# Optimization experiments

Measured on AMD Instinct MI355X. Metric: run time of the kernel, lower is better.

## Reference

```python
import jax, jax.numpy as jnp
import numpy as np

DIM = 1024
HEADS = 16
HEAD_DIM = DIM // HEADS
SCALE = HEAD_DIM ** -0.5


def setup_inputs() -> dict:
    key = jax.random.key(0)
    k1, k2, k3 = jax.random.split(key, 3)
    x = jax.random.normal(k1, (4, 2048, DIM), dtype=jnp.float32)
    # nn.Linear weight shape [out, in]; y = x @ W.T
    W_qkv = jax.random.normal(k2, (3 * DIM, DIM), dtype=jnp.float32) * (DIM ** -0.5)
    W_proj = jax.random.normal(k3, (DIM, DIM), dtype=jnp.float32) * (DIM ** -0.5)
    b_proj = jnp.zeros((DIM,), dtype=jnp.float32)
    return {"x": x, "W_qkv": W_qkv, "W_proj": W_proj, "b_proj": b_proj}


def reference(x, W_qkv, W_proj, b_proj):
    B, N, C = x.shape
    qkv = x @ W_qkv.T  # [B, N, 3C]
    qkv = qkv.reshape(B, N, 3, HEADS, HEAD_DIM).transpose(2, 0, 3, 1, 4)  # [3,B,H,N,D]
    q, k, v = qkv[0], qkv[1], qkv[2]
    attn = jnp.einsum('bhnd,bhmd->bhnm', q, k) * SCALE
    attn = jax.nn.softmax(attn, axis=-1)
    out = jnp.einsum('bhnm,bhmd->bhnd', attn, v)  # [B,H,N,D]
    out = out.transpose(0, 2, 1, 3).reshape(B, N, C)
    return out @ W_proj.T + b_proj
```

## Files before the change

kernel.cpp:

```cpp
#include <hip/hip_runtime.h>
#include <hip/hip_bf16.h>
#include <stdint.h>

typedef __attribute__((ext_vector_type(8))) __bf16 bf16x8;
typedef __attribute__((ext_vector_type(4))) float f32x4;
typedef __attribute__((ext_vector_type(16))) float f32x16;
typedef __attribute__((ext_vector_type(8))) unsigned short u16x8;
typedef __attribute__((ext_vector_type(4))) unsigned int u32x4;

#define DIM 1024
#define SEQ 2048
#define BATCH 4
#define MROWS (BATCH*SEQ)
#define QK_SCALE 0.1803368801111204f

__device__ __forceinline__ unsigned short f2bf(float f) {
  unsigned int u = __float_as_uint(f);
  u += 0x7fff + ((u >> 16) & 1);
  return (unsigned short)(u >> 16);
}

__device__ __forceinline__ void async16(const void* g, void* l) {
  __builtin_amdgcn_global_load_lds(
      (const __attribute__((address_space(1))) unsigned int*)g,
      (__attribute__((address_space(3))) unsigned int*)l, 16, 0, 0);
}

__device__ __forceinline__ unsigned cvtpk(float lo, float hi) {
  unsigned r;
  asm("v_cvt_pk_bf16_f32 %0, %1, %2" : "=v"(r) : "v"(lo), "v"(hi));
  return r;
}

__global__ __launch_bounds__(256) void cvt3(
    const float* __restrict__ x, const float* __restrict__ w1,
    const float* __restrict__ w2, unsigned short* __restrict__ xb,
    unsigned short* __restrict__ w1b, unsigned short* __restrict__ w2b) {
  const size_t NX = (size_t)MROWS * DIM;
  const size_t NW1 = (size_t)3 * DIM * DIM;
  const size_t NW2 = (size_t)DIM * DIM;
  size_t i = ((size_t)blockIdx.x * blockDim.x + threadIdx.x) * 8;
  const float* s; unsigned short* d; size_t off;
  if (i < NX) { s = x; d = xb; off = i; }
  else if (i < NX + NW1) { s = w1; d = w1b; off = i - NX; }
  else if (i < NX + NW1 + NW2) { s = w2; d = w2b; off = i - NX - NW1; }
  else return;
  float4 a = *(const float4*)(s + off);
  float4 b = *(const float4*)(s + off + 4);
  u16x8 r;
  r[0] = f2bf(a.x); r[1] = f2bf(a.y); r[2] = f2bf(a.z); r[3] = f2bf(a.w);
  r[4] = f2bf(b.x); r[5] = f2bf(b.y); r[6] = f2bf(b.z); r[7] = f2bf(b.w);
  *(u16x8*)(d + off) = r;
}

template<int OUT_BF16>
__global__ __launch_bounds__(256) void gemm_bt(
    const unsigned short* __restrict__ A, const unsigned short* __restrict__ Bt,
    unsigned short* __restrict__ Cb, float* __restrict__ Cf,
    const float* __restrict__ bias, int M, int N, int K,
    float qscale, int qcols)
{
  __shared__ unsigned short Asm[128 * 64];
  __shared__ unsigned short Bsm[128 * 64];

  int nwg = gridDim.x;
  int bid = blockIdx.x;
  int cpx = nwg >> 3;
  int wg = (bid & 7) * cpx + (bid >> 3);
  int ntn = N >> 7;
  int tn = wg % ntn, tm = wg / ntn;

  int t = threadIdx.x, l = t & 63, w = t >> 6;
  int lr = l & 15, lg = l >> 4;
  int wr = w >> 1, wc = w & 1;

  f32x4 acc[4][4] = {};

  const unsigned short* Ab = A + (size_t)tm * 128 * K;
  const unsigned short* Bb = Bt + (size_t)tn * 128 * K;

  for (int k0 = 0; k0 < K; k0 += 64) {
    #pragma unroll
    for (int i = 0; i < 4; ++i) {
      int idx = i * 256 + t;
      int row = idx >> 3, cc = (idx & 7) * 8;
      async16(Ab + (size_t)row * K + k0 + cc, (char*)Asm + idx * 16);
      async16(Bb + (size_t)row * K + k0 + cc, (char*)Bsm + idx * 16);
    }
    __syncthreads();
    #pragma unroll
    for (int kk = 0; kk < 2; ++kk) {
      bf16x8 af[4], bfr[4];
      #pragma unroll
      for (int m = 0; m < 4; ++m)
        af[m] = *(const bf16x8*)&Asm[(wr * 64 + m * 16 + lr) * 64 + kk * 32 + lg * 8];
      #pragma unroll
      for (int n = 0; n < 4; ++n)
        bfr[n] = *(const bf16x8*)&Bsm[(wc * 64 + n * 16 + lr) * 64 + kk * 32 + lg * 8];
      #pragma unroll
      for (int m = 0; m < 4; ++m)
        #pragma unroll
        for (int n = 0; n < 4; ++n)
          acc[m][n] = __builtin_amdgcn_mfma_f32_16x16x32_bf16(af[m], bfr[n], acc[m][n], 0, 0, 0);
    }
    __syncthreads();
  }

  #pragma unroll
  for (int m = 0; m < 4; ++m)
    #pragma unroll
    for (int n = 0; n < 4; ++n) {
      int col = tn * 128 + wc * 64 + n * 16 + lr;
      float cs = (OUT_BF16 && col < qcols) ? qscale : 1.0f;
      #pragma unroll
      for (int j = 0; j < 4; ++j) {
        int row = tm * 128 + wr * 64 + m * 16 + lg * 4 + j;
        if (OUT_BF16) Cb[(size_t)row * N + col] = f2bf(acc[m][n][j] * cs);
        else          Cf[(size_t)row * N + col] = acc[m][n][j] + bias[col];
      }
    }
}

__global__ __launch_bounds__(256, 4) void attn_fwd(
    const unsigned short* __restrict__ qkv, unsigned short* __restrict__ out)
{
  __shared__ unsigned short Ksm[2][64 * 64];
  __shared__ unsigned short Vt[2][64 * 64];
  __shared__ float bcast[4][32];

  const int bh = blockIdx.x;
  const int qt = blockIdx.y;
  const int b = bh >> 4, h = bh & 15;
  const int t = threadIdx.x, wid = t >> 6, l = t & 63;
  const int ql = l & 31, hi = l >> 5;

  const size_t RS = 3 * DIM;
  const unsigned short* base = qkv + (size_t)b * SEQ * RS + h * 64;
  const unsigned short* kb = base + DIM;
  const unsigned short* vp = base + 2 * DIM;

  const int qrow = qt * 128 + wid * 32 + ql;
  bf16x8 qf[4];
  #pragma unroll
  for (int s = 0; s < 4; ++s)
    qf[s] = *(const bf16x8*)(base + (size_t)qrow * RS + s * 16 + hi * 8);

  f32x16 oacc[2] = {};
  float rlp = 0.f;

  #define STAGE_K(KT, BUF)                                                   \
    _Pragma("unroll")                                                        \
    for (int i_ = 0; i_ < 2; ++i_) {                                         \
      int idx_ = i_ * 256 + t;                                               \
      int row_ = idx_ >> 3, pc_ = idx_ & 7;                                  \
      async16(kb + (size_t)((KT) * 64 + row_) * RS + (pc_ ^ (row_ & 7)) * 8, \
              (char*)(BUF) + idx_ * 16);                                     \
    }

  #define LOAD_V(KT, VA, VB)                                                 \
    {                                                                        \
      const unsigned short* p_ = vp + (size_t)((KT) * 64 + (t & 63)) * RS +  \
                                 (t >> 6) * 16;                              \
      VA = *(const u16x8*)p_;                                                \
      VB = *(const u16x8*)(p_ + 8);                                          \
    }

  #define WRITE_V(BUF, VA, VB)                                               \
    {                                                                        \
      int vn_ = t & 63, dg_ = t >> 6;                                        \
      int pc_ = (vn_ & 51) | ((vn_ & 4) << 1) | ((vn_ & 8) >> 1);            \
      _Pragma("unroll")                                                      \
      for (int j_ = 0; j_ < 8; ++j_) {                                       \
        int d0_ = dg_ * 16 + j_, d1_ = d0_ + 8;                              \
        (BUF)[d0_ * 64 + (((pc_ >> 3) ^ (d0_ & 7)) << 3) + (pc_ & 7)] = (VA)[j_]; \
        (BUF)[d1_ * 64 + (((pc_ >> 3) ^ (d1_ & 7)) << 3) + (pc_ & 7)] = (VB)[j_]; \
      }                                                                      \
    }

  {
    u16x8 va, vb2;
    STAGE_K(0, Ksm[0]);
    LOAD_V(0, va, vb2);
    WRITE_V(Vt[0], va, vb2);
  }
  __syncthreads();

  const int NT = SEQ / 64;
  int cur = 0;
  for (int kt = 0; kt < NT; ++kt) {
    u16x8 va, vb2;
    const bool pf = (kt + 1 < NT);
    if (pf) {
      STAGE_K(kt + 1, Ksm[cur ^ 1]);
      LOAD_V(kt + 1, va, vb2);
    }

    f32x16 st[2];
    __builtin_amdgcn_s_setprio(1);
    #pragma unroll
    for (int ti = 0; ti < 2; ++ti) {
      f32x16 a = {};
      int row = ti * 32 + ql;
      #pragma unroll
      for (int s = 0; s < 4; ++s) {
        bf16x8 af = *(const bf16x8*)&Ksm[cur][row * 64 + (((2 * s + hi) ^ (row & 7)) << 3)];
        a = __builtin_amdgcn_mfma_f32_32x32x16_bf16(af, qf[s], a, 0, 0, 0);
      }
      st[ti] = a;
    }
    __builtin_amdgcn_s_setprio(0);

    #pragma unroll
    for (int ti = 0; ti < 2; ++ti)
      #pragma unroll
      for (int r = 0; r < 16; ++r)
        st[ti][r] = __builtin_exp2f(st[ti][r]);
    float s0[8];
    #pragma unroll
    for (int r = 0; r < 8; ++r)
      s0[r] = (st[0][r] + st[0][r + 8]) + (st[1][r] + st[1][r + 8]);
    rlp += ((s0[0] + s0[1]) + (s0[2] + s0[3])) + ((s0[4] + s0[5]) + (s0[6] + s0[7]));

    bf16x8 pa[4];
    #pragma unroll
    for (int ti = 0; ti < 2; ++ti) {
      union { u32x4 u; bf16x8 v; } c0, c1;
      #pragma unroll
      for (int j = 0; j < 4; ++j) {
        c0.u[j] = cvtpk(st[ti][2 * j],     st[ti][2 * j + 1]);
        c1.u[j] = cvtpk(st[ti][8 + 2 * j], st[ti][8 + 2 * j + 1]);
      }
      pa[2 * ti]     = c0.v;
      pa[2 * ti + 1] = c1.v;
    }

    __builtin_amdgcn_s_setprio(1);
    #pragma unroll
    for (int c = 0; c < 4; ++c) {
      #pragma unroll
      for (int dh = 0; dh < 2; ++dh) {
        int row = dh * 32 + ql;
        bf16x8 vf = *(const bf16x8*)&Vt[cur][row * 64 + (((2 * c + hi) ^ (row & 7)) << 3)];
        oacc[dh] = __builtin_amdgcn_mfma_f32_32x32x16_bf16(pa[c], vf, oacc[dh], 0, 0, 0);
      }
    }
    __builtin_amdgcn_s_setprio(0);

    if (pf) { WRITE_V(Vt[cur ^ 1], va, vb2); }
    __syncthreads();
    cur ^= 1;
  }

  {
    float rl = rlp + __shfl_xor(rlp, 32);
    float inv = 1.0f / rl;
    if (l < 32) bcast[wid][l] = inv;
    asm volatile("s_waitcnt lgkmcnt(0)" ::: "memory");
    __builtin_amdgcn_sched_barrier(0);
    f32x4 ig[4];
    #pragma unroll
    for (int g = 0; g < 4; ++g)
      ig[g] = *(const f32x4*)&bcast[wid][8 * g + 4 * hi];
    #pragma unroll
    for (int dh = 0; dh < 2; ++dh) {
      #pragma unroll
      for (int g = 0; g < 4; ++g) {
        #pragma unroll
        for (int r2 = 0; r2 < 4; ++r2) {
          int q = r2 + 8 * g + 4 * hi;
          int grow = b * SEQ + qt * 128 + wid * 32 + q;
          int gcol = h * 64 + dh * 32 + ql;
          out[(size_t)grow * DIM + gcol] = f2bf(oacc[dh][g * 4 + r2] * ig[g][r2]);
        }
      }
    }
  }
  #undef STAGE_K
  #undef LOAD_V
  #undef WRITE_V
}

extern "C" void kernel_launch(void* const* d_in, const int* in_sizes, int n_in,
                              void* d_out, int out_size, void* d_ws, size_t ws_size,
                              hipStream_t stream) {
  const float* x     = (const float*)d_in[0];
  const float* Wqkv  = (const float*)d_in[1];
  const float* Wproj = (const float*)d_in[2];
  const float* bproj = (const float*)d_in[3];
  float* out = (float*)d_out;

  unsigned short* xb    = (unsigned short*)d_ws;
  unsigned short* w1b   = xb + (size_t)MROWS * DIM;
  unsigned short* w2b   = w1b + (size_t)3 * DIM * DIM;
  unsigned short* qkvb  = w2b + (size_t)DIM * DIM;
  unsigned short* attnb = qkvb + (size_t)MROWS * 3 * DIM;

  cvt3<<<6144, 256, 0, stream>>>(x, Wqkv, Wproj, xb, w1b, w2b);
  gemm_bt<1><<<(MROWS / 128) * (3 * DIM / 128), 256, 0, stream>>>(
      xb, w1b, qkvb, nullptr, nullptr, MROWS, 3 * DIM, DIM, QK_SCALE, DIM);
  attn_fwd<<<dim3(64, SEQ / 128), 256, 0, stream>>>(qkvb, attnb);
  gemm_bt<0><<<(MROWS / 128) * (DIM / 128), 256, 0, stream>>>(
      attnb, w2b, nullptr, out, bproj, MROWS, DIM, DIM, 1.0f, 0);
}
```

Before: 229.0 us.

## Software-pipeline attention loop: overlap next-tile QK MFMA with current softmax/PV

Restructures the attention inner loop into a two-stage software pipeline: each iteration computes QK^T scores for tile i while running exp, row-sum and PV for tile i-1. K and V staging moves to triple-buffered LDS so the prefetch runs two tiles ahead, and the loop is unrolled by two to alternate score registers. The intent is to hide exp and conversion latency behind MFMA work and to prefetch further ahead. In exchange, LDS use rises and launch bounds drop to 3 blocks per CU, which lowers occupancy and adds register pressure from holding two score tiles.

```diff
diff --git a/kernel.cpp b/kernel.cpp
--- a/kernel.cpp
+++ b/kernel.cpp
@@ -121,11 +121,11 @@
     }
 }
 
-__global__ __launch_bounds__(256, 4) void attn_fwd(
+__global__ __launch_bounds__(256, 3) void attn_fwd(
     const unsigned short* __restrict__ qkv, unsigned short* __restrict__ out)
 {
-  __shared__ unsigned short Ksm[2][64 * 64];
-  __shared__ unsigned short Vt[2][64 * 64];
+  __shared__ unsigned short Ksm[3][64 * 64];
+  __shared__ unsigned short Vt[3][64 * 64];
   __shared__ float bcast[4][32];
 
   const int bh = blockIdx.x;
@@ -146,7 +146,9 @@
     qf[s] = *(const bf16x8*)(base + (size_t)qrow * RS + s * 16 + hi * 8);
 
   f32x16 oacc[2] = {};
+  f32x16 stA[2], stB[2];
   float rlp = 0.f;
+  u16x8 va, vb2;
 
   #define STAGE_K(KT, BUF)                                                   \
     _Pragma("unroll")                                                        \
@@ -157,98 +159,118 @@
               (char*)(BUF) + idx_ * 16);                                     \
     }
 
-  #define LOAD_V(KT, VA, VB)                                                 \
+  #define LOAD_V(KT)                                                         \
     {                                                                        \
       const unsigned short* p_ = vp + (size_t)((KT) * 64 + (t & 63)) * RS +  \
                                  (t >> 6) * 16;                              \
-      VA = *(const u16x8*)p_;                                                \
-      VB = *(const u16x8*)(p_ + 8);                                          \
-    }
-
-  #define WRITE_V(BUF, VA, VB)                                               \
+      va = *(const u16x8*)p_;                                                \
+      vb2 = *(const u16x8*)(p_ + 8);                                         \
+    }
+
+  #define WRITE_V(BUF)                                                       \
     {                                                                        \
       int vn_ = t & 63, dg_ = t >> 6;                                        \
       int pc_ = (vn_ & 51) | ((vn_ & 4) << 1) | ((vn_ & 8) >> 1);            \
       _Pragma("unroll")                                                      \
       for (int j_ = 0; j_ < 8; ++j_) {                                       \
         int d0_ = dg_ * 16 + j_, d1_ = d0_ + 8;                              \
-        (BUF)[d0_ * 64 + (((pc_ >> 3) ^ (d0_ & 7)) << 3) + (pc_ & 7)] = (VA)[j_]; \
-        (BUF)[d1_ * 64 + (((pc_ >> 3) ^ (d1_ & 7)) << 3) + (pc_ & 7)] = (VB)[j_]; \
+        (BUF)[d0_ * 64 + (((pc_ >> 3) ^ (d0_ & 7)) << 3) + (pc_ & 7)] = va[j_]; \
+        (BUF)[d1_ * 64 + (((pc_ >> 3) ^ (d1_ & 7)) << 3) + (pc_ & 7)] = vb2[j_]; \
       }                                                                      \
     }
 
+  #define QK_MFMA(CUR, RBUF)                                                 \
+    __builtin_amdgcn_s_setprio(1);                                           \
+    _Pragma("unroll")                                                        \
+    for (int ti = 0; ti < 2; ++ti) {                                         \
+      f32x16 a_ = {};                                                        \
+      int row_ = ti * 32 + ql;                                               \
+      _Pragma("unroll")                                                      \
+      for (int s_ = 0; s_ < 4; ++s_) {                                       \
+        bf16x8 af_ = *(const bf16x8*)&(RBUF)[row_ * 64 +                     \
+                       (((2 * s_ + hi) ^ (row_ & 7)) << 3)];                 \
+        a_ = __builtin_amdgcn_mfma_f32_32x32x16_bf16(af_, qf[s_], a_, 0, 0, 0); \
+      }                                                                      \
+      CUR[ti] = a_;                                                          \
+    }                                                                        \
+    __builtin_amdgcn_s_setprio(0);
+
+  #define SM_PV(PRV, VBUF)                                                   \
+    {                                                                        \
+      _Pragma("unroll")                                                      \
+      for (int ti = 0; ti < 2; ++ti)                                         \
+        _Pragma("unroll")                                                    \
+        for (int rr = 0; rr < 16; ++rr)                                      \
+          PRV[ti][rr] = __builtin_exp2f(PRV[ti][rr]);                        \
+      float s0_[8];                                                          \
+      _Pragma("unroll")                                                      \
+      for (int rr = 0; rr < 8; ++rr)                                         \
+        s0_[rr] = (PRV[0][rr] + PRV[0][rr + 8]) + (PRV[1][rr] + PRV[1][rr + 8]); \
+      rlp += ((s0_[0] + s0_[1]) + (s0_[2] + s0_[3])) +                       \
+             ((s0_[4] + s0_[5]) + (s0_[6] + s0_[7]));                        \
+      bf16x8 pa_[4];                                                         \
+      _Pragma("unroll")                                                      \
+      for (int ti = 0; ti < 2; ++ti) {                                       \
+        union { u32x4 u; bf16x8 v; } c0_, c1_;                               \
+        _Pragma("unroll")                                                    \
+        for (int j_ = 0; j_ < 4; ++j_) {                                     \
+          c0_.u[j_] = cvtpk(PRV[ti][2 * j_],     PRV[ti][2 * j_ + 1]);       \
+          c1_.u[j_] = cvtpk(PRV[ti][8 + 2 * j_], PRV[ti][8 + 2 * j_ + 1]);   \
+        }                                                                    \
+        pa_[2 * ti] = c0_.v; pa_[2 * ti + 1] = c1_.v;                        \
+      }                                                                      \
+      __builtin_amdgcn_s_setprio(1);                                         \
+      _Pragma("unroll")                                                      \
+      for (int c_ = 0; c_ < 4; ++c_)                                         \
+        _Pragma("unroll")                                                    \
+        for (int dh_ = 0; dh_ < 2; ++dh_) {                                  \
+          int row_ = dh_ * 32 + ql;                                          \
+          bf16x8 vf_ = *(const bf16x8*)&(VBUF)[row_ * 64 +                   \
+                         (((2 * c_ + hi) ^ (row_ & 7)) << 3)];               \
+          oacc[dh_] = __builtin_amdgcn_mfma_f32_32x32x16_bf16(pa_[c_], vf_,  \
+                                                             oacc[dh_], 0, 0, 0); \
+        }                                                                    \
+      __builtin_amdgcn_s_setprio(0);                                         \
+    }
+
+  const int NT = SEQ / 64;
+
+  STAGE_K(0, Ksm[0]);
+  STAGE_K(1, Ksm[1]);
+  LOAD_V(0);
+  WRITE_V(Vt[0]);
+  LOAD_V(1);
+  __syncthreads();
+
+  STAGE_K(2, Ksm[2]);
+  WRITE_V(Vt[1]);
+  LOAD_V(2);
+  QK_MFMA(stA, Ksm[0]);
+  __syncthreads();
+
+  int r = 1;
+  #define BODY(I, CUR, PRV)                                                  \
+    {                                                                        \
+      int r2_ = r + 2; if (r2_ >= 3) r2_ -= 3;                               \
+      int r1_ = r + 1; if (r1_ >= 3) r1_ -= 3;                               \
+      if ((I) + 2 < NT) { STAGE_K((I) + 2, Ksm[r2_]); }                      \
+      if ((I) + 1 < NT) { WRITE_V(Vt[r1_]); }                                \
+      if ((I) + 2 < NT) { LOAD_V((I) + 2); }                                 \
+      QK_MFMA(CUR, Ksm[r]);                                                  \
+      SM_PV(PRV, Vt[r2_]);                                                   \
+      __syncthreads();                                                       \
+      r = r1_;                                                               \
+    }
+
+  for (int i = 1; i < NT - 1; i += 2) {
+    BODY(i, stB, stA);
+    BODY(i + 1, stA, stB);
+  }
+  BODY(NT - 1, stB, stA);
+
   {
-    u16x8 va, vb2;
-    STAGE_K(0, Ksm[0]);
-    LOAD_V(0, va, vb2);
-    WRITE_V(Vt[0], va, vb2);
-  }
-  __syncthreads();
-
-  const int NT = SEQ / 64;
-  int cur = 0;
-  for (int kt = 0; kt < NT; ++kt) {
-    u16x8 va, vb2;
-    const bool pf = (kt + 1 < NT);
-    if (pf) {
-      STAGE_K(kt + 1, Ksm[cur ^ 1]);
-      LOAD_V(kt + 1, va, vb2);
-    }
-
-    f32x16 st[2];
-    __builtin_amdgcn_s_setprio(1);
-    #pragma unroll
-    for (int ti = 0; ti < 2; ++ti) {
-      f32x16 a = {};
-      int row = ti * 32 + ql;
-      #pragma unroll
-      for (int s = 0; s < 4; ++s) {
-        bf16x8 af = *(const bf16x8*)&Ksm[cur][row * 64 + (((2 * s + hi) ^ (row & 7)) << 3)];
-        a = __builtin_amdgcn_mfma_f32_32x32x16_bf16(af, qf[s], a, 0, 0, 0);
-      }
-      st[ti] = a;
-    }
-    __builtin_amdgcn_s_setprio(0);
-
-    #pragma unroll
-    for (int ti = 0; ti < 2; ++ti)
-      #pragma unroll
-      for (int r = 0; r < 16; ++r)
-        st[ti][r] = __builtin_exp2f(st[ti][r]);
-    float s0[8];
-    #pragma unroll
-    for (int r = 0; r < 8; ++r)
-      s0[r] = (st[0][r] + st[0][r + 8]) + (st[1][r] + st[1][r + 8]);
-    rlp += ((s0[0] + s0[1]) + (s0[2] + s0[3])) + ((s0[4] + s0[5]) + (s0[6] + s0[7]));
-
-    bf16x8 pa[4];
-    #pragma unroll
-    for (int ti = 0; ti < 2; ++ti) {
-      union { u32x4 u; bf16x8 v; } c0, c1;
-      #pragma unroll
-      for (int j = 0; j < 4; ++j) {
-        c0.u[j] = cvtpk(st[ti][2 * j],     st[ti][2 * j + 1]);
-        c1.u[j] = cvtpk(st[ti][8 + 2 * j], st[ti][8 + 2 * j + 1]);
-      }
-      pa[2 * ti]     = c0.v;
-      pa[2 * ti + 1] = c1.v;
-    }
-
-    __builtin_amdgcn_s_setprio(1);
-    #pragma unroll
-    for (int c = 0; c < 4; ++c) {
-      #pragma unroll
-      for (int dh = 0; dh < 2; ++dh) {
-        int row = dh * 32 + ql;
-        bf16x8 vf = *(const bf16x8*)&Vt[cur][row * 64 + (((2 * c + hi) ^ (row & 7)) << 3)];
-        oacc[dh] = __builtin_amdgcn_mfma_f32_32x32x16_bf16(pa[c], vf, oacc[dh], 0, 0, 0);
-      }
-    }
-    __builtin_amdgcn_s_setprio(0);
-
-    if (pf) { WRITE_V(Vt[cur ^ 1], va, vb2); }
-    __syncthreads();
-    cur ^= 1;
+    int rv = r + 2; if (rv >= 3) rv -= 3;
+    SM_PV(stB, Vt[rv]);
   }
 
   {
@@ -278,6 +300,9 @@
   #undef STAGE_K
   #undef LOAD_V
   #undef WRITE_V
+  #undef QK_MFMA
+  #undef SM_PV
+  #undef BODY
 }
 
 extern "C" void kernel_launch(void* const* d_in, const int* in_sizes, int n_in,
```

Measured after the change: 276.0 us. 20.5% more time.

## Compute softmax row sums via MFMA with ones and precompute LDS addresses

Applied to the files above, without the earlier changes.

Replaces the per-tile scalar VALU reduction of the exponentiated scores with an extra MFMA against a ones vector. The row sums then land in the same register layout as the output accumulator, which removes the LDS broadcast and shuffle in the epilogue. It also hoists the swizzled LDS and global address computations out of the loop into precomputed offsets and uses a fast reciprocal. The cost is four more MFMAs per tile, a larger register footprint, and row sums taken from bf16-rounded probabilities rather than fp32 values.

```diff
diff --git a/kernel.cpp b/kernel.cpp
--- a/kernel.cpp
+++ b/kernel.cpp
@@ -126,7 +126,6 @@
 {
   __shared__ unsigned short Ksm[2][64 * 64];
   __shared__ unsigned short Vt[2][64 * 64];
-  __shared__ float bcast[4][32];
 
   const int bh = blockIdx.x;
   const int qt = blockIdx.y;
@@ -135,9 +134,23 @@
   const int ql = l & 31, hi = l >> 5;
 
   const size_t RS = 3 * DIM;
+  const int TSTRIDE = 64 * 3 * DIM;
   const unsigned short* base = qkv + (size_t)b * SEQ * RS + h * 64;
-  const unsigned short* kb = base + DIM;
-  const unsigned short* vp = base + 2 * DIM;
+
+  int rb[4];
+  #pragma unroll
+  for (int s = 0; s < 4; ++s)
+    rb[s] = ql * 64 + (((2 * s + hi) ^ (ql & 7)) << 3);
+  const int dg = t >> 6, vn = t & 63;
+  const int pcw = (vn & 51) | ((vn & 4) << 1) | ((vn & 8) >> 1);
+  int vw[8];
+  #pragma unroll
+  for (int j = 0; j < 8; ++j)
+    vw[j] = (dg * 16 + j) * 64 + (((pcw >> 3) ^ j) << 3) + (pcw & 7);
+  const int sk_src0 = (t >> 3) * (int)RS + ((t & 7) ^ ((t >> 3) & 7)) * 8;
+  const int sk_src1 = sk_src0 + 32 * (int)RS;
+  const int sk_dst = t * 16;
+  const int lv_src = vn * (int)RS + dg * 16;
 
   const int qrow = qt * 128 + wid * 32 + ql;
   bf16x8 qf[4];
@@ -145,54 +158,54 @@
   for (int s = 0; s < 4; ++s)
     qf[s] = *(const bf16x8*)(base + (size_t)qrow * RS + s * 16 + hi * 8);
 
+  bf16x8 ones;
+  {
+    union { u16x8 u; bf16x8 v; } o_;
+    #pragma unroll
+    for (int e = 0; e < 8; ++e) o_.u[e] = 0x3F80;
+    ones = o_.v;
+  }
+
   f32x16 oacc[2] = {};
-  float rlp = 0.f;
-
-  #define STAGE_K(KT, BUF)                                                   \
+  f32x16 racc = {};
+  u16x8 va, vb2;
+
+  const unsigned short* kpt = base + DIM;
+  const unsigned short* vpt = base + 2 * DIM;
+
+  #define STAGE_K(BUF)                                                       \
+    {                                                                        \
+      async16(kpt + sk_src0, (char*)(BUF) + sk_dst);                         \
+      async16(kpt + sk_src1, (char*)(BUF) + 4096 + sk_dst);                  \
+      kpt += TSTRIDE;                                                        \
+    }
+
+  #define LOAD_V()                                                           \
+    {                                                                        \
+      va  = *(const u16x8*)(vpt + lv_src);                                   \
+      vb2 = *(const u16x8*)(vpt + lv_src + 8);                               \
+      vpt += TSTRIDE;                                                        \
+    }
+
+  #define WRITE_V(BUF)                                                       \
     _Pragma("unroll")                                                        \
-    for (int i_ = 0; i_ < 2; ++i_) {                                         \
-      int idx_ = i_ * 256 + t;                                               \
-      int row_ = idx_ >> 3, pc_ = idx_ & 7;                                  \
-      async16(kb + (size_t)((KT) * 64 + row_) * RS + (pc_ ^ (row_ & 7)) * 8, \
-              (char*)(BUF) + idx_ * 16);                                     \
-    }
-
-  #define LOAD_V(KT, VA, VB)                                                 \
-    {                                                                        \
-      const unsigned short* p_ = vp + (size_t)((KT) * 64 + (t & 63)) * RS +  \
-                                 (t >> 6) * 16;                              \
-      VA = *(const u16x8*)p_;                                                \
-      VB = *(const u16x8*)(p_ + 8);                                          \
-    }
-
-  #define WRITE_V(BUF, VA, VB)                                               \
-    {                                                                        \
-      int vn_ = t & 63, dg_ = t >> 6;                                        \
-      int pc_ = (vn_ & 51) | ((vn_ & 4) << 1) | ((vn_ & 8) >> 1);            \
-      _Pragma("unroll")                                                      \
-      for (int j_ = 0; j_ < 8; ++j_) {                                       \
-        int d0_ = dg_ * 16 + j_, d1_ = d0_ + 8;                              \
-        (BUF)[d0_ * 64 + (((pc_ >> 3) ^ (d0_ & 7)) << 3) + (pc_ & 7)] = (VA)[j_]; \
-        (BUF)[d1_ * 64 + (((pc_ >> 3) ^ (d1_ & 7)) << 3) + (pc_ & 7)] = (VB)[j_]; \
-      }                                                                      \
-    }
-
-  {
-    u16x8 va, vb2;
-    STAGE_K(0, Ksm[0]);
-    LOAD_V(0, va, vb2);
-    WRITE_V(Vt[0], va, vb2);
-  }
+    for (int j_ = 0; j_ < 8; ++j_) {                                         \
+      (BUF)[vw[j_]]       = va[j_];                                          \
+      (BUF)[vw[j_] + 512] = vb2[j_];                                         \
+    }
+
+  STAGE_K(Ksm[0]);
+  LOAD_V();
+  WRITE_V(Vt[0]);
   __syncthreads();
 
   const int NT = SEQ / 64;
   int cur = 0;
   for (int kt = 0; kt < NT; ++kt) {
-    u16x8 va, vb2;
     const bool pf = (kt + 1 < NT);
     if (pf) {
-      STAGE_K(kt + 1, Ksm[cur ^ 1]);
-      LOAD_V(kt + 1, va, vb2);
+      STAGE_K(Ksm[cur ^ 1]);
+      LOAD_V();
     }
 
     f32x16 st[2];
@@ -200,10 +213,9 @@
     #pragma unroll
     for (int ti = 0; ti < 2; ++ti) {
       f32x16 a = {};
-      int row = ti * 32 + ql;
       #pragma unroll
       for (int s = 0; s < 4; ++s) {
-        bf16x8 af = *(const bf16x8*)&Ksm[cur][row * 64 + (((2 * s + hi) ^ (row & 7)) << 3)];
+        bf16x8 af = *(const bf16x8*)&Ksm[cur][ti * 2048 + rb[s]];
         a = __builtin_amdgcn_mfma_f32_32x32x16_bf16(af, qf[s], a, 0, 0, 0);
       }
       st[ti] = a;
@@ -215,11 +227,6 @@
       #pragma unroll
       for (int r = 0; r < 16; ++r)
         st[ti][r] = __builtin_exp2f(st[ti][r]);
-    float s0[8];
-    #pragma unroll
-    for (int r = 0; r < 8; ++r)
-      s0[r] = (st[0][r] + st[0][r + 8]) + (st[1][r] + st[1][r + 8]);
-    rlp += ((s0[0] + s0[1]) + (s0[2] + s0[3])) + ((s0[4] + s0[5]) + (s0[6] + s0[7]));
 
     bf16x8 pa[4];
     #pragma unroll
@@ -239,39 +246,30 @@
     for (int c = 0; c < 4; ++c) {
       #pragma unroll
       for (int dh = 0; dh < 2; ++dh) {
-        int row = dh * 32 + ql;
-        bf16x8 vf = *(const bf16x8*)&Vt[cur][row * 64 + (((2 * c + hi) ^ (row & 7)) << 3)];
+        bf16x8 vf = *(const bf16x8*)&Vt[cur][dh * 2048 + rb[c]];
         oacc[dh] = __builtin_amdgcn_mfma_f32_32x32x16_bf16(pa[c], vf, oacc[dh], 0, 0, 0);
       }
+      racc = __builtin_amdgcn_mfma_f32_32x32x16_bf16(pa[c], ones, racc, 0, 0, 0);
     }
     __builtin_amdgcn_s_setprio(0);
 
-    if (pf) { WRITE_V(Vt[cur ^ 1], va, vb2); }
+    if (pf) { WRITE_V(Vt[cur ^ 1]); }
     __syncthreads();
     cur ^= 1;
   }
 
   {
-    float rl = rlp + __shfl_xor(rlp, 32);
-    float inv = 1.0f / rl;
-    if (l < 32) bcast[wid][l] = inv;
-    asm volatile("s_waitcnt lgkmcnt(0)" ::: "memory");
-    __builtin_amdgcn_sched_barrier(0);
-    f32x4 ig[4];
-    #pragma unroll
-    for (int g = 0; g < 4; ++g)
-      ig[g] = *(const f32x4*)&bcast[wid][8 * g + 4 * hi];
-    #pragma unroll
-    for (int dh = 0; dh < 2; ++dh) {
-      #pragma unroll
-      for (int g = 0; g < 4; ++g) {
-        #pragma unroll
-        for (int r2 = 0; r2 < 4; ++r2) {
-          int q = r2 + 8 * g + 4 * hi;
-          int grow = b * SEQ + qt * 128 + wid * 32 + q;
-          int gcol = h * 64 + dh * 32 + ql;
-          out[(size_t)grow * DIM + gcol] = f2bf(oacc[dh][g * 4 + r2] * ig[g][r2]);
-        }
+    const int grow0 = b * SEQ + qt * 128 + wid * 32;
+    const int gcol0 = h * 64 + ql;
+    #pragma unroll
+    for (int g = 0; g < 4; ++g) {
+      #pragma unroll
+      for (int r2 = 0; r2 < 4; ++r2) {
+        float inv = __builtin_amdgcn_rcpf(racc[g * 4 + r2]);
+        int q = r2 + 8 * g + 4 * hi;
+        size_t rowoff = (size_t)(grow0 + q) * DIM + gcol0;
+        out[rowoff]      = f2bf(oacc[0][g * 4 + r2] * inv);
+        out[rowoff + 32] = f2bf(oacc[1][g * 4 + r2] * inv);
       }
     }
   }
```

Result: slower. 240.0 us (+4.8%).
